# Kernel optimization log

Hardware: AMD Instinct MI355X
Metric: run time of the kernel (lower is better)

## Reference

```python
import jax, jax.numpy as jnp
import numpy as np

B, N, C = 4, 4096, 1024
H, HC = 16, 64
R = int(HC * np.log(HC))  # 266 random features
EPS = 1e-3


def _orthogonal_projection(num_rows, num_cols, seed=0):
    # Block-orthogonal random matrix: QR of gaussian blocks, rows concatenated.
    rng = np.random.default_rng(seed)
    blocks = []
    n_full = num_rows // num_cols
    for _ in range(n_full):
        q, _ = np.linalg.qr(rng.standard_normal((num_cols, num_cols)))
        blocks.append(q.T)
    remain = num_rows - n_full * num_cols
    if remain > 0:
        q, _ = np.linalg.qr(rng.standard_normal((num_cols, num_cols)))
        blocks.append(q.T[:remain])
    return np.concatenate(blocks, axis=0).astype(np.float32)  # (num_rows, num_cols)


def setup_inputs() -> dict:
    key = jax.random.key(0)
    ks = jax.random.split(key, 6)
    scale = 0.02
    return {
        "x": jax.random.normal(ks[0], (B, N, C), dtype=jnp.float32),
        "Wq": jax.random.normal(ks[1], (C, H * HC), dtype=jnp.float32) * scale,
        "Wk": jax.random.normal(ks[2], (C, H * HC), dtype=jnp.float32) * scale,
        "Wv": jax.random.normal(ks[3], (C, H * HC), dtype=jnp.float32) * scale,
        "Wo": jax.random.normal(ks[4], (H * HC, C), dtype=jnp.float32) * scale,
        "bo": jnp.zeros((C,), dtype=jnp.float32),
        "proj": jnp.asarray(_orthogonal_projection(R, HC, seed=0)),
    }


def reference(x, Wq, Wk, Wv, Wo, bo, proj):
    b, n, _ = x.shape
    # qkv projections, split heads: (B, H, N, HC)
    q = (x @ Wq).reshape(b, n, H, HC).transpose(0, 2, 1, 3)
    k = (x @ Wk).reshape(b, n, H, HC).transpose(0, 2, 1, 3)
    v = (x @ Wv).reshape(b, n, H, HC).transpose(0, 2, 1, 3)
    # FAVOR+ generalized kernel: relu(x @ proj^T) + eps -> (B, H, N, R)
    qp = jax.nn.relu(jnp.einsum('bhnd,rd->bhnr', q, proj)) + EPS
    kp = jax.nn.relu(jnp.einsum('bhnd,rd->bhnr', k, proj)) + EPS
    # linear attention: O(N) in sequence length
    k_sum = kp.sum(axis=-2)                                   # (B, H, R)
    d_inv = 1.0 / jnp.einsum('bhnr,bhr->bhn', qp, k_sum)      # (B, H, N)
    kv = jnp.einsum('bhnr,bhnd->bhrd', kp, v)                 # (B, H, R, HC)
    qkv = jnp.einsum('bhnr,bhrd->bhnd', qp, kv)               # (B, H, N, HC)
    out = qkv * d_inv[..., None]
    # merge heads and output projection
    out = out.transpose(0, 2, 1, 3).reshape(b, n, H * HC)
    return out @ Wo + bo
```

## Files before the change

kernel.cpp:

```cpp
#include <hip/hip_runtime.h>
#include <hip/hip_bf16.h>


typedef __bf16 bf16x8 __attribute__((ext_vector_type(8)));
typedef unsigned short u16x8 __attribute__((ext_vector_type(8)));
typedef float  f32x4  __attribute__((ext_vector_type(4)));

#define EPS_F 1e-3f

__device__ __forceinline__ void gld16(const void* g, void* l) {
  __builtin_amdgcn_global_load_lds(
      (const __attribute__((address_space(1))) void*)g,
      (__attribute__((address_space(3))) void*)l, 16, 0, 0);
}

template <int EPI>
__global__ void __launch_bounds__(512, 2)
gemm256(const __hip_bfloat16* __restrict__ A, long lda,
        const __hip_bfloat16* __restrict__ Bt, long ldb,
        void* __restrict__ Cp, long ldc,
        int Mtiles, int Ntiles, int K, const float* __restrict__ bias) {
  __shared__ __align__(16) char sm[131072];

  const int tid  = threadIdx.x;
  const int lane = tid & 63;
  const int wave = tid >> 6;
  const int wm   = wave >> 2;
  const int wn   = wave & 3;
  const int quad = lane >> 4;
  const int l15  = lane & 15;

  const int bid = blockIdx.x;
  const int Mx  = Mtiles >> 3;
  const int xcd = bid & 7;
  const int wl  = bid >> 3;
  const int gsz = Mx << 2;
  const int grp = wl / gsz;
  const int rr  = wl - grp * gsz;
  const int mt  = xcd * Mx + (rr % Mx);
  const int nt  = (grp << 2) + (rr / Mx);
  const long m0 = (long)mt * 256;
  const long n0 = (long)nt * 256;

  const int srow = tid >> 3;
  const int sg   = (tid & 7) ^ (srow & 7);
  const __hip_bfloat16* aS = A  + (m0 + srow) * lda + sg * 8;
  const __hip_bfloat16* bS = Bt + (n0 + srow) * ldb + sg * 8;
  char* smc = (char*)sm;
  const int ldsOff = tid * 16;

  const int aRowB = (wm * 128 + l15) * 128;
  const int bRowB = 32768 + (wn * 64 + l15) * 128;
  const int sw    = (l15 & 7) << 4;
  const int cx0   = (quad * 16) ^ sw;
  const int cx1   = (64 + quad * 16) ^ sw;

  f32x4 acc[8][4] = {};

#define STAGE256(pp, kk)                                                     \
  {                                                                          \
    char* ab = smc + (pp) * 65536;                                           \
    _Pragma("unroll") for (int i = 0; i < 4; ++i) {                          \
      gld16(aS + (long)i * 64 * lda + (kk), ab + i * 8192 + ldsOff);         \
      gld16(bS + (long)i * 64 * ldb + (kk), ab + 32768 + i * 8192 + ldsOff); \
    }                                                                        \
  }

  const int NT = K >> 6;
  STAGE256(0, 0)
  STAGE256(1, 64)
  asm volatile("s_waitcnt vmcnt(8)" ::: "memory");
  __builtin_amdgcn_s_barrier();
  asm volatile("" ::: "memory");

  int p = 0;
  for (int t = 0; t < NT; ++t) {
    const char* base = smc + p * 65536;
    bf16x8 bfr[4][2];
#pragma unroll
    for (int jt = 0; jt < 4; ++jt) {
      bfr[jt][0] = *(const bf16x8*)(base + bRowB + jt * 2048 + cx0);
      bfr[jt][1] = *(const bf16x8*)(base + bRowB + jt * 2048 + cx1);
    }
    __builtin_amdgcn_s_setprio(1);
#pragma unroll
    for (int ih = 0; ih < 2; ++ih) {
      bf16x8 af[4][2];
#pragma unroll
      for (int it = 0; it < 4; ++it) {
        af[it][0] = *(const bf16x8*)(base + aRowB + (ih * 4 + it) * 2048 + cx0);
        af[it][1] = *(const bf16x8*)(base + aRowB + (ih * 4 + it) * 2048 + cx1);
      }
#pragma unroll
      for (int it = 0; it < 4; ++it)
#pragma unroll
        for (int jt = 0; jt < 4; ++jt) {
          acc[ih * 4 + it][jt] = __builtin_amdgcn_mfma_f32_16x16x32_bf16(
              af[it][0], bfr[jt][0], acc[ih * 4 + it][jt], 0, 0, 0);
          acc[ih * 4 + it][jt] = __builtin_amdgcn_mfma_f32_16x16x32_bf16(
              af[it][1], bfr[jt][1], acc[ih * 4 + it][jt], 0, 0, 0);
        }
    }
    __builtin_amdgcn_s_setprio(0);
    __builtin_amdgcn_s_barrier();
    asm volatile("" ::: "memory");
    if (t + 2 < NT) {
      STAGE256(p, (long)(t + 2) * 64)
      asm volatile("s_waitcnt vmcnt(8)" ::: "memory");
    } else {
      asm volatile("s_waitcnt vmcnt(0)" ::: "memory");
    }
    __builtin_amdgcn_s_barrier();
    asm volatile("" ::: "memory");
    p ^= 1;
  }
#undef STAGE256

  if constexpr (EPI == 7) {
    __hip_bfloat16* Cb = (__hip_bfloat16*)Cp;
    const long slab  = (n0 >> 10) * 16777216;
    const long ncol0 = (n0 & 1023) + wn * 64 + l15;
#pragma unroll
    for (int it = 0; it < 8; ++it) {
#pragma unroll
      for (int i = 0; i < 4; ++i) {
        const long gm = m0 + wm * 128 + it * 16 + quad * 4 + i;
        __hip_bfloat16* rowp = Cb + slab + gm * 1024 + ncol0;
#pragma unroll
        for (int jt = 0; jt < 4; ++jt)
          rowp[jt * 16] = (__hip_bfloat16)acc[it][jt][i];
      }
    }
  } else if constexpr (EPI == 5) {
    float* Cf = (float*)Cp;
    float bv[4];
#pragma unroll
    for (int jt = 0; jt < 4; ++jt)
      bv[jt] = bias[n0 + wn * 64 + jt * 16 + l15];
#pragma unroll
    for (int it = 0; it < 8; ++it) {
#pragma unroll
      for (int i = 0; i < 4; ++i) {
        const long gm = m0 + wm * 128 + it * 16 + quad * 4 + i;
        float* rowp = Cf + gm * ldc + n0 + wn * 64 + l15;
#pragma unroll
        for (int jt = 0; jt < 4; ++jt)
          rowp[jt * 16] = acc[it][jt][i] + bv[jt];
      }
    }
  }
}

__global__ void __launch_bounds__(512, 2)
favor_kv(const __hip_bfloat16* __restrict__ Kb,
         const __hip_bfloat16* __restrict__ Vb,
         const __hip_bfloat16* __restrict__ projb_g,
         float* __restrict__ kvp) {
  __shared__ __align__(16) char sm[147456];
  char* Kt = sm;
  char* Pj = sm + 16384;
  char* KP = sm + 53248;
  char* VT = sm + 126976;

  const int tid  = threadIdx.x;
  const int lane = tid & 63;
  const int wave = tid >> 6;
  const int quad = lane >> 4;
  const int l15  = lane & 15;
  const int swL  = (l15 & 7) << 4;

  const int bh   = blockIdx.x & 63;
  const int slab = blockIdx.x >> 6;
  const int b    = bh >> 4, h = bh & 15;
  const long rowbase = (long)b * 4096 + (long)slab * 1024;

  for (int p = 0; p < 5; ++p) {
    const int idx = p * 512 + tid;
    if (idx < 2304) {
      const int r = idx >> 3, g = (idx & 7) ^ (r & 7);
      gld16(projb_g + r * 64 + g * 8, Pj + p * 8192 + tid * 16);
    }
  }
  {
    unsigned short* vth = (unsigned short*)(VT + 64 * 256);
    const unsigned short one_bf = 0x3F80;
    for (int i = tid; i < 2048; i += 512) vth[i] = (i < 128) ? one_bf : 0;
  }

  const int rS = tid >> 3, gS = (tid & 7) ^ (rS & 7);
  const int rS2 = rS + 64, gS2 = (tid & 7) ^ (rS2 & 7);
  const int nl = tid >> 3, seg = tid & 7;
  gld16(Kb + (rowbase + rS) * 1024 + h * 64 + gS * 8, Kt + tid * 16);
  gld16(Kb + (rowbase + rS2) * 1024 + h * 64 + gS2 * 8, Kt + 8192 + tid * 16);
  u16x8 vc0 = *(const u16x8*)(Vb + (rowbase + nl) * 1024 + h * 64 + seg * 8);
  u16x8 vc1 =
      *(const u16x8*)(Vb + (rowbase + 64 + nl) * 1024 + h * 64 + seg * 8);

  const int wm1 = wave & 3;
  const int wn1 = wave >> 2;
  const int nJ = (wave < 2) ? 3 : 2;

  f32x4 acc2[3][5] = {};

  for (int t = 0; t < 8; ++t) {
    asm volatile("s_waitcnt vmcnt(0)" ::: "memory");
    __builtin_amdgcn_s_barrier();
    asm volatile("" ::: "memory");
    {
#pragma unroll
      for (int j = 0; j < 8; ++j) {
        const int d = seg * 8 + j;
        const int s = ((d & 7) ^ ((d >> 3) & 7)) << 4;
        *(unsigned short*)(VT + d * 256 + ((nl * 2) ^ s)) = vc0[j];
        *(unsigned short*)(VT + d * 256 + (((nl + 64) * 2) ^ s)) = vc1[j];
      }
    }
    f32x4 acc1[2][9] = {};
#pragma unroll
    for (int ks = 0; ks < 2; ++ks) {
      const int cb = ks * 64 + quad * 16;
      bf16x8 af[2];
#pragma unroll
      for (int fm = 0; fm < 2; ++fm)
        af[fm] = *(const bf16x8*)(Kt + (wm1 * 32 + fm * 16 + l15) * 128 +
                                  (cb ^ swL));
      bf16x8 bfr[9];
#pragma unroll
      for (int fn = 0; fn < 9; ++fn)
        bfr[fn] = *(const bf16x8*)(Pj + (wn1 * 144 + fn * 16 + l15) * 128 +
                                   (cb ^ swL));
#pragma unroll
      for (int fm = 0; fm < 2; ++fm)
#pragma unroll
        for (int fn = 0; fn < 9; ++fn)
          acc1[fm][fn] = __builtin_amdgcn_mfma_f32_16x16x32_bf16(
              af[fm], bfr[fn], acc1[fm][fn], 0, 0, 0);
    }
#pragma unroll
    for (int fm = 0; fm < 2; ++fm) {
      const int nb = (wm1 * 32 + fm * 16 + quad * 4) * 2;
#pragma unroll
      for (int fn = 0; fn < 9; ++fn) {
        const int r = wn1 * 144 + fn * 16 + l15;
        const bool ok = (r < 266);
        union { __hip_bfloat16 hh[4]; uint2 u; } pk;
#pragma unroll
        for (int ii = 0; ii < 4; ++ii) {
          float v = acc1[fm][fn][ii];
          v = ok ? (fmaxf(v, 0.f) + EPS_F) : 0.f;
          pk.hh[ii] = (__hip_bfloat16)v;
        }
        *(uint2*)(KP + r * 256 + (nb ^ ((r & 7) << 4))) = pk.u;
      }
    }
    asm volatile("s_waitcnt lgkmcnt(0)" ::: "memory");
    __builtin_amdgcn_s_barrier();
    asm volatile("" ::: "memory");
    if (t < 7) {
      const long n1 = (long)(t + 1) * 128;
      gld16(Kb + (rowbase + n1 + rS) * 1024 + h * 64 + gS * 8, Kt + tid * 16);
      gld16(Kb + (rowbase + n1 + rS2) * 1024 + h * 64 + gS2 * 8,
            Kt + 8192 + tid * 16);
      vc0 = *(const u16x8*)(Vb + (rowbase + n1 + nl) * 1024 + h * 64 +
                            seg * 8);
      vc1 = *(const u16x8*)(Vb + (rowbase + n1 + 64 + nl) * 1024 + h * 64 +
                            seg * 8);
    }
#pragma unroll
    for (int ks = 0; ks < 4; ++ks) {
      const int cb = ks * 64 + quad * 16;
      bf16x8 bfr[5];
#pragma unroll
      for (int fd = 0; fd < 5; ++fd) {
        const int d = fd * 16 + l15;
        const int s = ((d & 7) ^ ((d >> 3) & 7)) << 4;
        bfr[fd] = *(const bf16x8*)(VT + d * 256 + (cb ^ s));
      }
#pragma unroll
      for (int j = 0; j < 3; ++j) {
        if (j < nJ) {
          const int r = (wave + 8 * j) * 16 + l15;
          const bf16x8 af =
              *(const bf16x8*)(KP + r * 256 + (cb ^ ((r & 7) << 4)));
#pragma unroll
          for (int fd = 0; fd < 5; ++fd)
            acc2[j][fd] = __builtin_amdgcn_mfma_f32_16x16x32_bf16(
                af, bfr[fd], acc2[j][fd], 0, 0, 0);
        }
      }
    }
  }
  float* dst = kvp + (long)blockIdx.x * 23040;
#pragma unroll
  for (int j = 0; j < 3; ++j) {
    if (j < nJ) {
      const int rb = (wave + 8 * j) * 16 + quad * 4;
#pragma unroll
      for (int fd = 0; fd < 5; ++fd) {
        const int d = fd * 16 + l15;
#pragma unroll
        for (int ii = 0; ii < 4; ++ii)
          dst[(long)(rb + ii) * 80 + d] = acc2[j][fd][ii];
      }
    }
  }
}

__global__ void __launch_bounds__(256)
finalize_kvx2(const float* __restrict__ kvp,
              __hip_bfloat16* __restrict__ kvxb) {
  __shared__ float lds_f[23040];
  const int bh = blockIdx.x, t = threadIdx.x;
  for (int p = 0; p < 90; ++p) {
    const int idx = p * 256 + t;
    float s = 0.f;
#pragma unroll
    for (int sl = 0; sl < 4; ++sl)
      s += kvp[(long)(sl * 64 + bh) * 23040 + idx];
    lds_f[idx] = s;
  }
  __syncthreads();
  for (int p = 0; p < 90; ++p) {
    const int idx = p * 256 + t;
    const int d = idx / 288, r = idx % 288;
    kvxb[(long)bh * 23040 + idx] = (__hip_bfloat16)lds_f[r * 80 + d];
  }
}

__global__ void __launch_bounds__(512, 2)
favor_out(const __hip_bfloat16* __restrict__ Qb,
          const __hip_bfloat16* __restrict__ kvxb_g,
          const __hip_bfloat16* __restrict__ projb_g,
          __hip_bfloat16* __restrict__ outm) {
  __shared__ __align__(16) char sm[160512];
  char* Pj = sm;
  char* KX = sm + 36864;
  char* QP = sm + 84224;
  float* Dsh = (float*)(sm + 160000);

  const int tid  = threadIdx.x;
  const int lane = tid & 63;
  const int wave = tid >> 6;
  const int quad = lane >> 4;
  const int l15  = lane & 15;
  const int swL  = (l15 & 7) << 4;

  const int bh  = blockIdx.x >> 3;
  const int rb8 = blockIdx.x & 7;
  const int b = bh >> 4, h = bh & 15;
  const long rowbase = (long)b * 4096 + (long)rb8 * 512;

  for (int p = 0; p < 5; ++p) {
    const int idx = p * 512 + tid;
    if (idx < 2304) {
      const int r = idx >> 3, g = (idx & 7) ^ (r & 7);
      gld16(projb_g + r * 64 + g * 8, Pj + p * 8192 + tid * 16);
    }
  }
  {
    const __hip_bfloat16* src = kvxb_g + (long)bh * 23040;
#pragma unroll
    for (int p = 0; p < 6; ++p) {
      const int idx = p * 512 + tid;
      if (idx < 2880) {
        const int d = idx / 36, g = idx % 36;
        const bf16x8 v = *(const bf16x8*)(src + d * 288 + g * 8);
        *(bf16x8*)(KX + d * 592 + g * 16) = v;
      }
    }
  }
  const int rS = tid >> 3, gS = (tid & 7) ^ (rS & 7);
  const int rS2 = rS + 64, gS2 = (tid & 7) ^ (rS2 & 7);
  u16x8 qv0 = *(const u16x8*)(Qb + (rowbase + rS) * 1024 + h * 64 + gS * 8);
  u16x8 qv1 = *(const u16x8*)(Qb + (rowbase + rS2) * 1024 + h * 64 + gS2 * 8);

  const int wm1 = wave >> 2;
  const int wn1 = wave & 3;

  for (int s = 0; s < 4; ++s) {
    *(u16x8*)(QP + tid * 16) = qv0;
    *(u16x8*)(QP + 8192 + tid * 16) = qv1;
    asm volatile("s_waitcnt lgkmcnt(0)" ::: "memory");
    if (s == 0) asm volatile("s_waitcnt vmcnt(0)" ::: "memory");
    __builtin_amdgcn_s_barrier();
    asm volatile("" ::: "memory");
    f32x4 acc1[9][2] = {};
#pragma unroll
    for (int ks = 0; ks < 2; ++ks) {
      const int cb = ks * 64 + quad * 16;
      bf16x8 bfr[2];
#pragma unroll
      for (int fn = 0; fn < 2; ++fn)
        bfr[fn] = *(const bf16x8*)(QP + (wn1 * 32 + fn * 16 + l15) * 128 +
                                   (cb ^ swL));
      bf16x8 af[9];
#pragma unroll
      for (int fm = 0; fm < 9; ++fm)
        af[fm] = *(const bf16x8*)(Pj + (wm1 * 144 + fm * 16 + l15) * 128 +
                                  (cb ^ swL));
#pragma unroll
      for (int fm = 0; fm < 9; ++fm)
#pragma unroll
        for (int fn = 0; fn < 2; ++fn)
          acc1[fm][fn] = __builtin_amdgcn_mfma_f32_16x16x32_bf16(
              af[fm], bfr[fn], acc1[fm][fn], 0, 0, 0);
    }
    if (s < 3) {
      const long n1 = (long)(s + 1) * 128;
      qv0 = *(const u16x8*)(Qb + (rowbase + n1 + rS) * 1024 + h * 64 + gS * 8);
      qv1 = *(const u16x8*)(Qb + (rowbase + n1 + rS2) * 1024 + h * 64 +
                            gS2 * 8);
    }
    __builtin_amdgcn_s_barrier();
    asm volatile("" ::: "memory");
#pragma unroll
    for (int fm = 0; fm < 9; ++fm) {
      const int r0 = wm1 * 144 + fm * 16 + quad * 4;
#pragma unroll
      for (int fn = 0; fn < 2; ++fn) {
        const int n = wn1 * 32 + fn * 16 + l15;
        union { __hip_bfloat16 hh[4]; uint2 u; } pk;
#pragma unroll
        for (int ii = 0; ii < 4; ++ii) {
          float v = acc1[fm][fn][ii];
          v = (r0 + ii < 266) ? (fmaxf(v, 0.f) + EPS_F) : 0.f;
          pk.hh[ii] = (__hip_bfloat16)v;
        }
        *(uint2*)(QP + n * 592 + r0 * 2) = pk.u;
      }
    }
    asm volatile("s_waitcnt lgkmcnt(0)" ::: "memory");
    __builtin_amdgcn_s_barrier();
    asm volatile("" ::: "memory");
    f32x4 acc2[5] = {};
#pragma unroll
    for (int ks = 0; ks < 9; ++ks) {
      const int cb = ks * 64 + quad * 16;
      const bf16x8 af = *(const bf16x8*)(QP + (wave * 16 + l15) * 592 + cb);
      bf16x8 bfr[5];
#pragma unroll
      for (int fd = 0; fd < 5; ++fd)
        bfr[fd] = *(const bf16x8*)(KX + (fd * 16 + l15) * 592 + cb);
#pragma unroll
      for (int fd = 0; fd < 5; ++fd)
        acc2[fd] = __builtin_amdgcn_mfma_f32_16x16x32_bf16(af, bfr[fd],
                                                           acc2[fd], 0, 0, 0);
    }
    if (l15 == 0) {
#pragma unroll
      for (int ii = 0; ii < 4; ++ii)
        Dsh[wave * 16 + quad * 4 + ii] = acc2[4][ii];
    }
    asm volatile("s_waitcnt lgkmcnt(0)" ::: "memory");
    __builtin_amdgcn_s_barrier();
    asm volatile("" ::: "memory");
#pragma unroll
    for (int ii = 0; ii < 4; ++ii) {
      const int nloc = wave * 16 + quad * 4 + ii;
      const float den = Dsh[nloc];
      const float dinv = (den > 1e-30f) ? (1.f / den) : 0.f;
      __hip_bfloat16* rowp =
          outm + (rowbase + (long)s * 128 + nloc) * 1024 + h * 64;
#pragma unroll
      for (int fd = 0; fd < 4; ++fd)
        rowp[fd * 16 + l15] = (__hip_bfloat16)(acc2[fd][ii] * dinv);
    }
  }
}

__global__ void cvt_x(const float* __restrict__ x,
                      __hip_bfloat16* __restrict__ xb) {
  const long i = ((long)blockIdx.x * 256 + threadIdx.x) * 8;
  const float4 f0 = *(const float4*)(x + i);
  const float4 f1 = *(const float4*)(x + i + 4);
  union { __hip_bfloat16 h[8]; uint4 u; } r;
  r.h[0] = (__hip_bfloat16)f0.x; r.h[1] = (__hip_bfloat16)f0.y;
  r.h[2] = (__hip_bfloat16)f0.z; r.h[3] = (__hip_bfloat16)f0.w;
  r.h[4] = (__hip_bfloat16)f1.x; r.h[5] = (__hip_bfloat16)f1.y;
  r.h[6] = (__hip_bfloat16)f1.z; r.h[7] = (__hip_bfloat16)f1.w;
  *(uint4*)(xb + i) = r.u;
}

__global__ void transpose_w4(const float* __restrict__ s0,
                             const float* __restrict__ s1,
                             const float* __restrict__ s2,
                             const float* __restrict__ s3,
                             __hip_bfloat16* __restrict__ dq,
                             __hip_bfloat16* __restrict__ dwo) {
  __shared__ float t[32][33];
  const int z = blockIdx.z;
  const float* src = (z == 0) ? s0 : (z == 1) ? s1 : (z == 2) ? s2 : s3;
  __hip_bfloat16* dst = (z < 3) ? (dq + (long)z * 1048576) : dwo;
  const int k0 = blockIdx.x * 32, n0 = blockIdx.y * 32;
  const int tx = threadIdx.x & 31, ty = threadIdx.x >> 5;
#pragma unroll
  for (int i = 0; i < 4; ++i)
    t[ty + i * 8][tx] = src[(long)(k0 + ty + i * 8) * 1024 + n0 + tx];
  __syncthreads();
#pragma unroll
  for (int i = 0; i < 4; ++i)
    dst[(long)(n0 + ty + i * 8) * 1024 + k0 + tx] =
        (__hip_bfloat16)t[tx][ty + i * 8];
}

__global__ void prep_proj(const float* __restrict__ proj,
                          __hip_bfloat16* __restrict__ projb) {
  const int i = blockIdx.x * 256 + threadIdx.x;
  if (i < 288 * 64) {
    const int r = i >> 6;
    __hip_bfloat16 v = (__hip_bfloat16)0.f;
    if (r < 266) v = (__hip_bfloat16)proj[i];
    projb[i] = v;
  }
}

extern "C" void kernel_launch(void* const* d_in, const int* in_sizes, int n_in,
                              void* d_out, int out_size, void* d_ws,
                              size_t ws_size, hipStream_t stream) {
  const float* x    = (const float*)d_in[0];
  const float* Wq   = (const float*)d_in[1];
  const float* Wk   = (const float*)d_in[2];
  const float* Wv   = (const float*)d_in[3];
  const float* Wo   = (const float*)d_in[4];
  const float* bo   = (const float*)d_in[5];
  const float* proj = (const float*)d_in[6];
  float* out = (float*)d_out;
  char* ws = (char*)d_ws;

  constexpr long o_wqkvt = 0;
  constexpr long o_wot   = 6291456;
  constexpr long o_projb = 8388608;
  constexpr long o_Qb    = 8425472;
  constexpr long o_Kb    = 41979904;
  constexpr long o_Vb    = 75534336;
  constexpr long o_xb    = 109088768;
  constexpr long o_kvp   = 109088768;
  constexpr long o_kvxb  = 132681728;

  __hip_bfloat16* wqkvt = (__hip_bfloat16*)(ws + o_wqkvt);
  __hip_bfloat16* wot   = (__hip_bfloat16*)(ws + o_wot);
  __hip_bfloat16* projb = (__hip_bfloat16*)(ws + o_projb);
  __hip_bfloat16* Qb    = (__hip_bfloat16*)(ws + o_Qb);
  __hip_bfloat16* Kb    = (__hip_bfloat16*)(ws + o_Kb);
  __hip_bfloat16* Vb    = (__hip_bfloat16*)(ws + o_Vb);
  __hip_bfloat16* xb    = (__hip_bfloat16*)(ws + o_xb);
  float*          kvp   = (float*)(ws + o_kvp);
  __hip_bfloat16* kvxb  = (__hip_bfloat16*)(ws + o_kvxb);
  __hip_bfloat16* outm  = Kb;

  cvt_x<<<8192, 256, 0, stream>>>(x, xb);
  transpose_w4<<<dim3(32, 32, 4), 256, 0, stream>>>(Wq, Wk, Wv, Wo, wqkvt,
                                                    wot);
  prep_proj<<<72, 256, 0, stream>>>(proj, projb);

  gemm256<7><<<768, 512, 0, stream>>>(xb, 1024, wqkvt, 1024, Qb, 0, 64, 12,
                                      1024, nullptr);

  favor_kv<<<256, 512, 0, stream>>>(Kb, Vb, projb, kvp);
  finalize_kvx2<<<64, 256, 0, stream>>>(kvp, kvxb);

  favor_out<<<512, 512, 0, stream>>>(Qb, kvxb, projb, outm);

  gemm256<5><<<256, 512, 0, stream>>>(outm, 1024, wot, 1024, out, 1024, 64, 4,
                                      1024, bo);
}
```

Measured before the change: 387.4 us.

## Interleave global prefetch with four-quadrant MFMA phases in 256x256 GEMM loop

Splits each K-step of the 256x256 bf16 GEMM main loop into four quadrant phases, each with its own LDS fragment loads, barrier and MFMA block. Global-to-LDS prefetch for step t+2 is now split into small groups and issued into the same buffer as soon as the A/B rows it overwrites have been read into registers, instead of all at once after the full compute. The aim is to spread memory traffic across the iteration and overlap LDS reads with MFMA work. In exchange it adds more barriers per iteration and relies on subtle row-ownership reasoning to avoid overwriting LDS data that is still needed.

New measurement: 387.1 us. About the same (-0.1%).

```diff
diff --git a/kernel.cpp b/kernel.cpp
--- a/kernel.cpp
+++ b/kernel.cpp
@@ -57,18 +57,18 @@
 
   f32x4 acc[8][4] = {};
 
-#define STAGE256(pp, kk)                                                     \
-  {                                                                          \
-    char* ab = smc + (pp) * 65536;                                           \
-    _Pragma("unroll") for (int i = 0; i < 4; ++i) {                          \
-      gld16(aS + (long)i * 64 * lda + (kk), ab + i * 8192 + ldsOff);         \
-      gld16(bS + (long)i * 64 * ldb + (kk), ab + 32768 + i * 8192 + ldsOff); \
-    }                                                                        \
-  }
+#define GLD_A(pp, kk, i)                                                   \
+  gld16(aS + (long)(i) * 64 * lda + (kk),                                  \
+        smc + (pp) * 65536 + (i) * 8192 + ldsOff);
+#define GLD_B(pp, kk, i)                                                   \
+  gld16(bS + (long)(i) * 64 * ldb + (kk),                                  \
+        smc + (pp) * 65536 + 32768 + (i) * 8192 + ldsOff);
 
   const int NT = K >> 6;
-  STAGE256(0, 0)
-  STAGE256(1, 64)
+#pragma unroll
+  for (int i = 0; i < 4; ++i) { GLD_A(0, 0, i) GLD_B(0, 0, i) }
+#pragma unroll
+  for (int i = 0; i < 4; ++i) { GLD_A(1, 64, i) GLD_B(1, 64, i) }
   asm volatile("s_waitcnt vmcnt(8)" ::: "memory");
   __builtin_amdgcn_s_barrier();
   asm volatile("" ::: "memory");
@@ -76,36 +76,98 @@
   int p = 0;
   for (int t = 0; t < NT; ++t) {
     const char* base = smc + p * 65536;
-    bf16x8 bfr[4][2];
-#pragma unroll
-    for (int jt = 0; jt < 4; ++jt) {
-      bfr[jt][0] = *(const bf16x8*)(base + bRowB + jt * 2048 + cx0);
-      bfr[jt][1] = *(const bf16x8*)(base + bRowB + jt * 2048 + cx1);
-    }
+    const long kk = (long)(t + 2) * 64;
+    const bool pf = (t + 2 < NT);
+    bf16x8 af[4][2], b01[2][2], b23[2][2];
+
+#pragma unroll
+    for (int it = 0; it < 4; ++it) {
+      af[it][0] = *(const bf16x8*)(base + aRowB + it * 2048 + cx0);
+      af[it][1] = *(const bf16x8*)(base + aRowB + it * 2048 + cx1);
+    }
+#pragma unroll
+    for (int jt = 0; jt < 2; ++jt) {
+      b01[jt][0] = *(const bf16x8*)(base + bRowB + jt * 2048 + cx0);
+      b01[jt][1] = *(const bf16x8*)(base + bRowB + jt * 2048 + cx1);
+    }
+    asm volatile("" ::: "memory");
+    __builtin_amdgcn_s_barrier();
+    asm volatile("s_waitcnt lgkmcnt(0)" ::: "memory");
     __builtin_amdgcn_s_setprio(1);
 #pragma unroll
-    for (int ih = 0; ih < 2; ++ih) {
-      bf16x8 af[4][2];
-#pragma unroll
-      for (int it = 0; it < 4; ++it) {
-        af[it][0] = *(const bf16x8*)(base + aRowB + (ih * 4 + it) * 2048 + cx0);
-        af[it][1] = *(const bf16x8*)(base + aRowB + (ih * 4 + it) * 2048 + cx1);
-      }
-#pragma unroll
-      for (int it = 0; it < 4; ++it)
-#pragma unroll
-        for (int jt = 0; jt < 4; ++jt) {
-          acc[ih * 4 + it][jt] = __builtin_amdgcn_mfma_f32_16x16x32_bf16(
-              af[it][0], bfr[jt][0], acc[ih * 4 + it][jt], 0, 0, 0);
-          acc[ih * 4 + it][jt] = __builtin_amdgcn_mfma_f32_16x16x32_bf16(
-              af[it][1], bfr[jt][1], acc[ih * 4 + it][jt], 0, 0, 0);
-        }
-    }
+    for (int it = 0; it < 4; ++it)
+#pragma unroll
+      for (int jt = 0; jt < 2; ++jt) {
+        acc[it][jt] = __builtin_amdgcn_mfma_f32_16x16x32_bf16(
+            af[it][0], b01[jt][0], acc[it][jt], 0, 0, 0);
+        acc[it][jt] = __builtin_amdgcn_mfma_f32_16x16x32_bf16(
+            af[it][1], b01[jt][1], acc[it][jt], 0, 0, 0);
+      }
     __builtin_amdgcn_s_setprio(0);
     __builtin_amdgcn_s_barrier();
     asm volatile("" ::: "memory");
-    if (t + 2 < NT) {
-      STAGE256(p, (long)(t + 2) * 64)
+
+#pragma unroll
+    for (int jt = 0; jt < 2; ++jt) {
+      b23[jt][0] = *(const bf16x8*)(base + bRowB + (jt + 2) * 2048 + cx0);
+      b23[jt][1] = *(const bf16x8*)(base + bRowB + (jt + 2) * 2048 + cx1);
+    }
+    if (pf) { GLD_A(p, kk, 0) GLD_A(p, kk, 2) }
+    asm volatile("" ::: "memory");
+    __builtin_amdgcn_s_barrier();
+    asm volatile("s_waitcnt lgkmcnt(0)" ::: "memory");
+    __builtin_amdgcn_s_setprio(1);
+#pragma unroll
+    for (int it = 0; it < 4; ++it)
+#pragma unroll
+      for (int jt = 0; jt < 2; ++jt) {
+        acc[it][jt + 2] = __builtin_amdgcn_mfma_f32_16x16x32_bf16(
+            af[it][0], b23[jt][0], acc[it][jt + 2], 0, 0, 0);
+        acc[it][jt + 2] = __builtin_amdgcn_mfma_f32_16x16x32_bf16(
+            af[it][1], b23[jt][1], acc[it][jt + 2], 0, 0, 0);
+      }
+    __builtin_amdgcn_s_setprio(0);
+    __builtin_amdgcn_s_barrier();
+    asm volatile("" ::: "memory");
+
+#pragma unroll
+    for (int it = 0; it < 4; ++it) {
+      af[it][0] = *(const bf16x8*)(base + aRowB + (4 + it) * 2048 + cx0);
+      af[it][1] = *(const bf16x8*)(base + aRowB + (4 + it) * 2048 + cx1);
+    }
+    if (pf) { GLD_B(p, kk, 0) GLD_B(p, kk, 1) GLD_B(p, kk, 2) }
+    asm volatile("" ::: "memory");
+    __builtin_amdgcn_s_barrier();
+    asm volatile("s_waitcnt lgkmcnt(0)" ::: "memory");
+    __builtin_amdgcn_s_setprio(1);
+#pragma unroll
+    for (int it = 0; it < 4; ++it)
+#pragma unroll
+      for (int jt = 0; jt < 2; ++jt) {
+        acc[4 + it][jt + 2] = __builtin_amdgcn_mfma_f32_16x16x32_bf16(
+            af[it][0], b23[jt][0], acc[4 + it][jt + 2], 0, 0, 0);
+        acc[4 + it][jt + 2] = __builtin_amdgcn_mfma_f32_16x16x32_bf16(
+            af[it][1], b23[jt][1], acc[4 + it][jt + 2], 0, 0, 0);
+      }
+    __builtin_amdgcn_s_setprio(0);
+    __builtin_amdgcn_s_barrier();
+    asm volatile("" ::: "memory");
+
+    if (pf) { GLD_B(p, kk, 3) GLD_A(p, kk, 1) GLD_A(p, kk, 3) }
+    asm volatile("" ::: "memory");
+    __builtin_amdgcn_s_barrier();
+    __builtin_amdgcn_s_setprio(1);
+#pragma unroll
+    for (int it = 0; it < 4; ++it)
+#pragma unroll
+      for (int jt = 0; jt < 2; ++jt) {
+        acc[4 + it][jt] = __builtin_amdgcn_mfma_f32_16x16x32_bf16(
+            af[it][0], b01[jt][0], acc[4 + it][jt], 0, 0, 0);
+        acc[4 + it][jt] = __builtin_amdgcn_mfma_f32_16x16x32_bf16(
+            af[it][1], b01[jt][1], acc[4 + it][jt], 0, 0, 0);
+      }
+    __builtin_amdgcn_s_setprio(0);
+    if (pf) {
       asm volatile("s_waitcnt vmcnt(8)" ::: "memory");
     } else {
       asm volatile("s_waitcnt vmcnt(0)" ::: "memory");
@@ -114,7 +176,8 @@
     asm volatile("" ::: "memory");
     p ^= 1;
   }
-#undef STAGE256
+#undef GLD_A
+#undef GLD_B
 
   if constexpr (EPI == 7) {
     __hip_bfloat16* Cb = (__hip_bfloat16*)Cp;
```

## Interleave LDS fragment loads with MFMA clusters and overlap prefetch with compute

Applied to the files above, without the earlier changes.

Restructures the 256x256 GEMM main loop into eight MFMA clusters, with LDS fragment reads for the next cluster issued between them. The global-to-LDS prefetch is now issued before the last two clusters, and the first fragments of the next tile are loaded early. This is meant to hide LDS read latency and barrier stalls behind matrix-core work. It raises register pressure from the double-buffered fragment sets and makes the synchronisation ordering more intricate.

After: 380.0 us. Within noise of the previous version (-1.9%).

```diff
diff --git a/kernel.cpp b/kernel.cpp
--- a/kernel.cpp
+++ b/kernel.cpp
@@ -57,64 +57,100 @@
 
   f32x4 acc[8][4] = {};
 
-#define STAGE256(pp, kk)                                                     \
-  {                                                                          \
-    char* ab = smc + (pp) * 65536;                                           \
-    _Pragma("unroll") for (int i = 0; i < 4; ++i) {                          \
-      gld16(aS + (long)i * 64 * lda + (kk), ab + i * 8192 + ldsOff);         \
-      gld16(bS + (long)i * 64 * ldb + (kk), ab + 32768 + i * 8192 + ldsOff); \
-    }                                                                        \
-  }
+#define GLD_A(pp, kk, i)                                                   \
+  gld16(aS + (long)(i) * 64 * lda + (kk),                                  \
+        smc + (pp) * 65536 + (i) * 8192 + ldsOff);
+#define GLD_B(pp, kk, i)                                                   \
+  gld16(bS + (long)(i) * 64 * ldb + (kk),                                  \
+        smc + (pp) * 65536 + 32768 + (i) * 8192 + ldsOff);
+
+#define QCL(AR, BR, accI, accJ)                                            \
+  __builtin_amdgcn_s_setprio(1);                                           \
+  _Pragma("unroll") for (int it = 0; it < 4; ++it)                         \
+      _Pragma("unroll") for (int jt = 0; jt < 2; ++jt)                     \
+          acc[(accI) + it][(accJ) + jt] =                                  \
+              __builtin_amdgcn_mfma_f32_16x16x32_bf16(                     \
+                  AR[it], BR[jt], acc[(accI) + it][(accJ) + jt], 0, 0, 0); \
+  __builtin_amdgcn_s_setprio(0);
 
   const int NT = K >> 6;
-  STAGE256(0, 0)
-  STAGE256(1, 64)
+#pragma unroll
+  for (int i = 0; i < 4; ++i) { GLD_A(0, 0, i) GLD_B(0, 0, i) }
+#pragma unroll
+  for (int i = 0; i < 4; ++i) { GLD_A(1, 64, i) GLD_B(1, 64, i) }
   asm volatile("s_waitcnt vmcnt(8)" ::: "memory");
   __builtin_amdgcn_s_barrier();
   asm volatile("" ::: "memory");
 
+  bf16x8 a0k0[4], a1k0[4], a0k1[4], a1k1[4];
+  bf16x8 b01k0[2], b23k0[2], b01k1[2], b23k1[2];
+#pragma unroll
+  for (int jt = 0; jt < 2; ++jt)
+    b01k0[jt] = *(const bf16x8*)(smc + bRowB + jt * 2048 + cx0);
+#pragma unroll
+  for (int it = 0; it < 4; ++it)
+    a0k0[it] = *(const bf16x8*)(smc + aRowB + it * 2048 + cx0);
+
   int p = 0;
   for (int t = 0; t < NT; ++t) {
-    const char* base = smc + p * 65536;
-    bf16x8 bfr[4][2];
-#pragma unroll
-    for (int jt = 0; jt < 4; ++jt) {
-      bfr[jt][0] = *(const bf16x8*)(base + bRowB + jt * 2048 + cx0);
-      bfr[jt][1] = *(const bf16x8*)(base + bRowB + jt * 2048 + cx1);
-    }
-    __builtin_amdgcn_s_setprio(1);
-#pragma unroll
-    for (int ih = 0; ih < 2; ++ih) {
-      bf16x8 af[4][2];
-#pragma unroll
-      for (int it = 0; it < 4; ++it) {
-        af[it][0] = *(const bf16x8*)(base + aRowB + (ih * 4 + it) * 2048 + cx0);
-        af[it][1] = *(const bf16x8*)(base + aRowB + (ih * 4 + it) * 2048 + cx1);
-      }
-#pragma unroll
-      for (int it = 0; it < 4; ++it)
-#pragma unroll
-        for (int jt = 0; jt < 4; ++jt) {
-          acc[ih * 4 + it][jt] = __builtin_amdgcn_mfma_f32_16x16x32_bf16(
-              af[it][0], bfr[jt][0], acc[ih * 4 + it][jt], 0, 0, 0);
-          acc[ih * 4 + it][jt] = __builtin_amdgcn_mfma_f32_16x16x32_bf16(
-              af[it][1], bfr[jt][1], acc[ih * 4 + it][jt], 0, 0, 0);
-        }
-    }
-    __builtin_amdgcn_s_setprio(0);
-    __builtin_amdgcn_s_barrier();
-    asm volatile("" ::: "memory");
-    if (t + 2 < NT) {
-      STAGE256(p, (long)(t + 2) * 64)
+    const char* base  = smc + p * 65536;
+    const char* nbase = smc + (p ^ 1) * 65536;
+    const long kk = (long)(t + 2) * 64;
+    const bool pf = (t + 2 < NT);
+
+#pragma unroll
+    for (int jt = 0; jt < 2; ++jt)
+      b23k0[jt] = *(const bf16x8*)(base + bRowB + (jt + 2) * 2048 + cx0);
+    QCL(a0k0, b01k0, 0, 0)
+#pragma unroll
+    for (int it = 0; it < 4; ++it)
+      a1k0[it] = *(const bf16x8*)(base + aRowB + (4 + it) * 2048 + cx0);
+    QCL(a0k0, b23k0, 0, 2)
+#pragma unroll
+    for (int jt = 0; jt < 2; ++jt)
+      b01k1[jt] = *(const bf16x8*)(base + bRowB + jt * 2048 + cx1);
+#pragma unroll
+    for (int it = 0; it < 4; ++it)
+      a0k1[it] = *(const bf16x8*)(base + aRowB + it * 2048 + cx1);
+    QCL(a1k0, b01k0, 4, 0)
+#pragma unroll
+    for (int jt = 0; jt < 2; ++jt)
+      b23k1[jt] = *(const bf16x8*)(base + bRowB + (jt + 2) * 2048 + cx1);
+    QCL(a1k0, b23k0, 4, 2)
+#pragma unroll
+    for (int it = 0; it < 4; ++it)
+      a1k1[it] = *(const bf16x8*)(base + aRowB + (4 + it) * 2048 + cx1);
+    QCL(a0k1, b01k1, 0, 0)
+    QCL(a0k1, b23k1, 0, 2)
+    asm volatile("s_waitcnt lgkmcnt(0)" ::: "memory");
+    __builtin_amdgcn_s_barrier();
+    asm volatile("" ::: "memory");
+    if (pf) {
+      GLD_A(p, kk, 0) GLD_A(p, kk, 1) GLD_A(p, kk, 2) GLD_A(p, kk, 3)
+      GLD_B(p, kk, 0) GLD_B(p, kk, 1) GLD_B(p, kk, 2) GLD_B(p, kk, 3)
+    }
+    QCL(a1k1, b01k1, 4, 0)
+    if (pf) {
       asm volatile("s_waitcnt vmcnt(8)" ::: "memory");
     } else {
       asm volatile("s_waitcnt vmcnt(0)" ::: "memory");
     }
     __builtin_amdgcn_s_barrier();
     asm volatile("" ::: "memory");
+    if (t + 1 < NT) {
+#pragma unroll
+      for (int jt = 0; jt < 2; ++jt)
+        b01k0[jt] = *(const bf16x8*)(nbase + bRowB + jt * 2048 + cx0);
+#pragma unroll
+      for (int it = 0; it < 4; ++it)
+        a0k0[it] = *(const bf16x8*)(nbase + aRowB + it * 2048 + cx0);
+    }
+    QCL(a1k1, b23k1, 4, 2)
     p ^= 1;
   }
-#undef STAGE256
+#undef GLD_A
+#undef GLD_B
+#undef QCL
 
   if constexpr (EPI == 7) {
     __hip_bfloat16* Cb = (__hip_bfloat16*)Cp;
```
